# Kernel optimization log

Hardware: AMD Instinct MI355X
Metric: run time of the kernel (lower is better)

## Reference

```python
import jax, jax.numpy as jnp
import numpy as np


def _make_coord(n):
    # grid-center coords in (-1, 1), matching make_coord in the torch code
    return -1.0 + 1.0 / n + (2.0 / n) * jnp.arange(n, dtype=jnp.float32)


def _mlp(inp, W1, b1, W2, b2, W3, b3):
    h = jax.nn.relu(inp @ W1 + b1)
    h = jax.nn.relu(h @ W2 + b2)
    return h @ W3 + b3


def setup_inputs() -> dict:
    key = jax.random.key(0)
    ks = jax.random.split(key, 4)
    dim = 64
    x = jax.random.normal(ks[0], (4, dim, 64, 64), dtype=jnp.float32)
    W1 = jax.random.normal(ks[1], (dim + 2, 256), dtype=jnp.float32) * 0.05
    W2 = jax.random.normal(ks[2], (256, 256), dtype=jnp.float32) * 0.05
    W3 = jax.random.normal(ks[3], (256, dim), dtype=jnp.float32) * 0.05
    return {
        "x": x,
        "W1": W1, "b1": jnp.zeros((256,), jnp.float32),
        "W2": W2, "b2": jnp.zeros((256,), jnp.float32),
        "W3": W3, "b3": jnp.zeros((dim,), jnp.float32),
        "h_out": 256, "w_out": 256,
    }


def reference(x, W1, b1, W2, b2, W3, b3, h_out, w_out):
    B, C, H, W = x.shape
    # query coords on the output grid (same for every batch element)
    gy, gx = jnp.meshgrid(_make_coord(h_out), _make_coord(w_out), indexing="ij")
    cy = gy.reshape(-1)  # [Q], coord channel 0 (height)
    cx = gx.reshape(-1)  # [Q], coord channel 1 (width)
    rx = 1.0 / H  # = 2 / H / 2
    ry = 1.0 / W
    eps_shift = 1e-6
    lim = 1.0 - 1e-6
    fy = _make_coord(H)  # feat_coord values along height
    fx = _make_coord(W)

    preds = []
    areas = []
    for vx in (-1.0, 1.0):
        for vy in (-1.0, 1.0):
            sy = jnp.clip(cy + vx * rx + eps_shift, -lim, lim)
            sx = jnp.clip(cx + vy * ry + eps_shift, -lim, lim)
            # grid_sample nearest, align_corners=False: unnormalize then round
            iy = jnp.clip(jnp.round(((sy + 1.0) * H - 1.0) * 0.5), 0, H - 1).astype(jnp.int32)
            ix = jnp.clip(jnp.round(((sx + 1.0) * W - 1.0) * 0.5), 0, W - 1).astype(jnp.int32)
            q_feat = x[:, :, iy, ix].transpose(0, 2, 1)  # [B, Q, C]
            rel_y = (cy - fy[iy]) * H  # [Q]
            rel_x = (cx - fx[ix]) * W
            rel = jnp.stack([rel_y, rel_x], axis=-1)  # [Q, 2]
            inp = jnp.concatenate(
                [q_feat, jnp.broadcast_to(rel, (B,) + rel.shape)], axis=-1
            )  # [B, Q, C+2]
            preds.append(_mlp(inp, W1, b1, W2, b2, W3, b3))  # [B, Q, C]
            areas.append(jnp.abs(rel_y * rel_x) + 1e-9)  # [Q]

    tot_area = areas[0] + areas[1] + areas[2] + areas[3]
    # local_ensemble swap: 0<->3, 1<->2 (opposite-corner area weighting)
    areas = [areas[3], areas[2], areas[1], areas[0]]
    ret = 0.0
    for pred, area in zip(preds, areas):
        ret = ret + pred * (area / tot_area)[None, :, None]
    return ret  # [B, h_out*w_out, C]
```

## Files before the change

### kernel.cpp

```cpp
#include <hip/hip_runtime.h>


typedef __bf16 bf16x8 __attribute__((ext_vector_type(8)));
typedef float  f32x4  __attribute__((ext_vector_type(4)));

#define LDS_SWZ(row, kbyte) ((kbyte) ^ (((row) & 7) << 4))

#define WP1_U 0
#define WP2_U (48 * 512)
#define WP3_U (176 * 512)

__global__ __launch_bounds__(64) void prep_weights(
    const float* __restrict__ W1, const float* __restrict__ W2,
    const float* __restrict__ W3, ushort* __restrict__ ws)
{
    const int blk = blockIdx.x;
    const int l   = threadIdx.x;
    const float* W; int Kreal, N, ks, nt; size_t off;
    if (blk < 48)       { W = W1; Kreal = 66;  N = 256; ks = blk >> 4;  nt = blk & 15; off = WP1_U + (size_t)blk * 512; }
    else if (blk < 176) { int b2 = blk - 48;  W = W2; Kreal = 256; N = 256; ks = b2 >> 4; nt = b2 & 15; off = WP2_U + (size_t)b2 * 512; }
    else                { int b3 = blk - 176; W = W3; Kreal = 256; N = 64;  ks = b3 >> 2; nt = b3 & 3;  off = WP3_U + (size_t)b3 * 512; }

    const int n = nt * 16 + (l & 15);
    ushort v[8];
    #pragma unroll
    for (int j = 0; j < 8; ++j) {
        const int k = ks * 32 + ((l >> 4) * 8) + j;
        const float f = (k < Kreal) ? W[(size_t)k * N + n] : 0.0f;
        v[j] = __builtin_bit_cast(ushort, (__bf16)f);
    }
    *(uint4*)(ws + off + (size_t)l * 8) = *(const uint4*)v;
}

template<int KSTEPS, int SRC_STRIDE>
__device__ inline void compute_layer(const char* __restrict__ src,
                                     const ushort* __restrict__ wp,
                                     const float* __restrict__ bias,
                                     int lane, int nbase_t, f32x4 (&acc)[4][4])
{
    const int lrow = lane & 15;
    const int lk   = lane >> 4;
    #pragma unroll
    for (int nt = 0; nt < 4; ++nt) {
        const float bs = bias[(nbase_t + nt) * 16 + lrow];
        #pragma unroll
        for (int mt = 0; mt < 4; ++mt)
            acc[mt][nt] = (f32x4){bs, bs, bs, bs};
    }

    const ushort* wpl = wp + (((size_t)nbase_t) << 9) + (lane << 3);
    #pragma unroll 1
    for (int ks = 0; ks < KSTEPS; ++ks) {
        bf16x8 bb[4];
        #pragma unroll
        for (int nt = 0; nt < 4; ++nt)
            bb[nt] = *(const bf16x8*)(wpl + (((size_t)(ks * 16 + nt)) << 9));
        #pragma unroll
        for (int mt = 0; mt < 4; ++mt) {
            const int row   = mt * 16 + lrow;
            const int kbyte = ks * 64 + lk * 16;
            const bf16x8 a = *(const bf16x8*)(src + row * SRC_STRIDE + LDS_SWZ(row, kbyte));
            __builtin_amdgcn_s_setprio(1);
            #pragma unroll
            for (int nt = 0; nt < 4; ++nt)
                acc[mt][nt] = __builtin_amdgcn_mfma_f32_16x16x32_bf16(a, bb[nt], acc[mt][nt], 0, 0, 0);
            __builtin_amdgcn_s_setprio(0);
        }
    }
}

__device__ inline void store_hidden(char* __restrict__ dst, const f32x4 (&acc)[4][4],
                                    int lane, int nbase_t)
{
    const int lrow = lane & 15;
    const int lk   = lane >> 4;
    #pragma unroll
    for (int nt = 0; nt < 4; ++nt) {
        const int n  = (nbase_t + nt) * 16 + lrow;
        const int kbyte = 2 * n;
        #pragma unroll
        for (int mt = 0; mt < 4; ++mt) {
            #pragma unroll
            for (int r = 0; r < 4; ++r) {
                const int row = mt * 16 + lk * 4 + r;
                const float v = fmaxf(acc[mt][nt][r], 0.0f);
                *(ushort*)(dst + row * 512 + LDS_SWZ(row, kbyte)) = __builtin_bit_cast(ushort, (__bf16)v);
            }
        }
    }
}

__global__ __launch_bounds__(256, 3) void liif_mfma4_kernel(
    const float* __restrict__ x,
    const float* __restrict__ b1f, const float* __restrict__ b2f, const float* __restrict__ b3f,
    const ushort* __restrict__ ws, float* __restrict__ out)
{
    __shared__ char bufI[16 * 1024];
    __shared__ char bufH[32 * 1024];
    __shared__ int   s_iy[4][16], s_ix[4][16];
    __shared__ float s_rely[4][16], s_relx[4][16], s_w[4][16];

    const int tid  = threadIdx.x;
    const int lane = tid & 63;
    const int wv   = tid >> 6;
    const int lrow = lane & 15;
    const int lk   = lane >> 4;

    const int bid0 = blockIdx.x;
    const int bid  = (bid0 & 7) * 2048 + (bid0 >> 3);
    const int b    = bid >> 12;
    const int q0   = (bid & 4095) << 4;

    const int nbase_t = wv * 4;

    if (tid < 16) {
        const int q  = q0 + tid;
        const int yq = q >> 8, xq = q & 255;
        const float cy  = -1.0f + (2.0f * yq + 1.0f) / 256.0f;
        const float cx  = -1.0f + (2.0f * xq + 1.0f) / 256.0f;
        const float lim = 1.0f - 1e-6f;
        float area[4];
        #pragma unroll
        for (int c = 0; c < 4; ++c) {
            const float vx = (c & 2) ? 1.0f : -1.0f;
            const float vy = (c & 1) ? 1.0f : -1.0f;
            float sy = cy + vx * (1.0f / 64.0f) + 1e-6f;
            float sx = cx + vy * (1.0f / 64.0f) + 1e-6f;
            sy = fminf(fmaxf(sy, -lim), lim);
            sx = fminf(fmaxf(sx, -lim), lim);
            int iy = (int)rintf(((sy + 1.0f) * 64.0f - 1.0f) * 0.5f);
            int ix = (int)rintf(((sx + 1.0f) * 64.0f - 1.0f) * 0.5f);
            iy = min(max(iy, 0), 63);
            ix = min(max(ix, 0), 63);
            const float fy = -1.0f + (2.0f * iy + 1.0f) / 64.0f;
            const float fx = -1.0f + (2.0f * ix + 1.0f) / 64.0f;
            const float ry = (cy - fy) * 64.0f;
            const float rx = (cx - fx) * 64.0f;
            s_iy[c][tid] = iy;   s_ix[c][tid] = ix;
            s_rely[c][tid] = ry; s_relx[c][tid] = rx;
            area[c] = fabsf(ry * rx) + 1e-9f;
        }
        const float tot = area[0] + area[1] + area[2] + area[3];
        #pragma unroll
        for (int c = 0; c < 4; ++c) s_w[c][tid] = area[3 - c] / tot;
    }
    __syncthreads();

    {
        const int r = tid >> 2, p = tid & 3;
        const int c = r >> 4, q = r & 15;
        const int iy = s_iy[c][q], ix = s_ix[c][q];
        const float* xb = x + (size_t)b * 262144 + iy * 64 + ix;
        #pragma unroll
        for (int half = 0; half < 2; ++half) {
            ushort tmp[8];
            #pragma unroll
            for (int j = 0; j < 8; ++j) {
                const float f = xb[(size_t)(p * 16 + half * 8 + j) * 4096];
                tmp[j] = __builtin_bit_cast(ushort, (__bf16)f);
            }
            const int kbyte = p * 32 + half * 16;
            *(uint4*)(bufI + r * 256 + LDS_SWZ(r, kbyte)) = *(const uint4*)tmp;
        }
        ushort pad[8] = {0, 0, 0, 0, 0, 0, 0, 0};
        if (p == 0) {
            pad[0] = __builtin_bit_cast(ushort, (__bf16)s_rely[c][q]);
            pad[1] = __builtin_bit_cast(ushort, (__bf16)s_relx[c][q]);
        }
        const int kbyte = 128 + p * 16;
        *(uint4*)(bufI + r * 256 + LDS_SWZ(r, kbyte)) = *(const uint4*)pad;
    }
    __syncthreads();

    f32x4 acc[4][4];

    compute_layer<3, 256>(bufI, ws + WP1_U, b1f, lane, nbase_t, acc);
    store_hidden(bufH, acc, lane, nbase_t);
    __syncthreads();

    compute_layer<8, 512>(bufH, ws + WP2_U, b2f, lane, nbase_t, acc);
    __syncthreads();
    store_hidden(bufH, acc, lane, nbase_t);
    __syncthreads();

    {
        const int nt3 = wv;
        const float bs = b3f[nt3 * 16 + lrow];
        f32x4 acc3[4];
        #pragma unroll
        for (int mt = 0; mt < 4; ++mt) acc3[mt] = (f32x4){bs, bs, bs, bs};

        const ushort* wp3 = ws + WP3_U + (lane << 3);
        #pragma unroll 1
        for (int ks = 0; ks < 8; ++ks) {
            const bf16x8 bb = *(const bf16x8*)(wp3 + (((size_t)(ks * 4 + nt3)) << 9));
            #pragma unroll
            for (int mt = 0; mt < 4; ++mt) {
                const int row   = mt * 16 + lrow;
                const int kbyte = ks * 64 + lk * 16;
                const bf16x8 a = *(const bf16x8*)(bufH + row * 512 + LDS_SWZ(row, kbyte));
                __builtin_amdgcn_s_setprio(1);
                acc3[mt] = __builtin_amdgcn_mfma_f32_16x16x32_bf16(a, bb, acc3[mt], 0, 0, 0);
                __builtin_amdgcn_s_setprio(0);
            }
        }
        #pragma unroll
        for (int mt = 0; mt < 4; ++mt) {
            #pragma unroll
            for (int r = 0; r < 4; ++r) {
                const int row = mt * 16 + lk * 4 + r;
                const float wgt = s_w[row >> 4][row & 15];
                const int cb = (nt3 * 16 + lrow) * 4;
                *(float*)(bufI + row * 256 + LDS_SWZ(row, cb)) = acc3[mt][r] * wgt;
            }
        }
    }
    __syncthreads();

    {
        const int q  = tid >> 4;
        const int ch = (tid & 15) * 4;
        f32x4 sum = (f32x4){0.f, 0.f, 0.f, 0.f};
        #pragma unroll
        for (int c = 0; c < 4; ++c) {
            const int row = c * 16 + q;
            const f32x4 v = *(const f32x4*)(bufI + row * 256 + LDS_SWZ(row, ch * 4));
            sum += v;
        }
        *(f32x4*)(out + ((size_t)b * 65536 + q0 + q) * 64 + ch) = sum;
    }
}

extern "C" void kernel_launch(void* const* d_in, const int* in_sizes, int n_in,
                              void* d_out, int out_size, void* d_ws, size_t ws_size,
                              hipStream_t stream) {
    const float* x  = (const float*)d_in[0];
    const float* W1 = (const float*)d_in[1];
    const float* b1 = (const float*)d_in[2];
    const float* W2 = (const float*)d_in[3];
    const float* b2 = (const float*)d_in[4];
    const float* W3 = (const float*)d_in[5];
    const float* b3 = (const float*)d_in[6];
    float* out = (float*)d_out;
    ushort* wp = (ushort*)d_ws;

    prep_weights<<<208, 64, 0, stream>>>(W1, W2, W3, wp);
    liif_mfma4_kernel<<<16384, 256, 0, stream>>>(x, b1, b2, b3, wp, out);
}
```

Baseline: 269.8 us.

## Pre-transpose features to pixel-major bf16 and load layer-1 A directly from global

Adds a prep kernel that converts x into a channel-contiguous bf16 layout per pixel, so the main kernel reads layer-1 A fragments straight from global memory instead of gathering strided fp32 values into shared memory. The relative-coordinate channels are injected directly into the A register for the last K-step, and the per-query coordinate math moves into registers. This removes the input LDS buffer, which together with a higher occupancy hint aims at more resident blocks. The cost is an extra prep pass and an extra barrier before reusing the hidden buffer for the output reduction.

```diff
diff --git a/kernel.cpp b/kernel.cpp
--- a/kernel.cpp
+++ b/kernel.cpp
@@ -9,6 +9,7 @@
 #define WP1_U 0
 #define WP2_U (48 * 512)
 #define WP3_U (176 * 512)
+#define XT_OFF (1 << 20)
 
 __global__ __launch_bounds__(64) void prep_weights(
     const float* __restrict__ W1, const float* __restrict__ W2,
@@ -32,41 +33,21 @@
     *(uint4*)(ws + off + (size_t)l * 8) = *(const uint4*)v;
 }
 
-template<int KSTEPS, int SRC_STRIDE>
-__device__ inline void compute_layer(const char* __restrict__ src,
-                                     const ushort* __restrict__ wp,
-                                     const float* __restrict__ bias,
-                                     int lane, int nbase_t, f32x4 (&acc)[4][4])
-{
-    const int lrow = lane & 15;
-    const int lk   = lane >> 4;
+__global__ __launch_bounds__(256) void prep_xt(const float* __restrict__ x, char* __restrict__ xt)
+{
+    const int blk = blockIdx.x;
+    const int b = blk >> 6, iy = blk & 63;
+    const int ix = threadIdx.x & 63, cq = threadIdx.x >> 6;
+    ushort v[16];
     #pragma unroll
-    for (int nt = 0; nt < 4; ++nt) {
-        const float bs = bias[(nbase_t + nt) * 16 + lrow];
-        #pragma unroll
-        for (int mt = 0; mt < 4; ++mt)
-            acc[mt][nt] = (f32x4){bs, bs, bs, bs};
-    }
-
-    const ushort* wpl = wp + (((size_t)nbase_t) << 9) + (lane << 3);
-    #pragma unroll 1
-    for (int ks = 0; ks < KSTEPS; ++ks) {
-        bf16x8 bb[4];
-        #pragma unroll
-        for (int nt = 0; nt < 4; ++nt)
-            bb[nt] = *(const bf16x8*)(wpl + (((size_t)(ks * 16 + nt)) << 9));
-        #pragma unroll
-        for (int mt = 0; mt < 4; ++mt) {
-            const int row   = mt * 16 + lrow;
-            const int kbyte = ks * 64 + lk * 16;
-            const bf16x8 a = *(const bf16x8*)(src + row * SRC_STRIDE + LDS_SWZ(row, kbyte));
-            __builtin_amdgcn_s_setprio(1);
-            #pragma unroll
-            for (int nt = 0; nt < 4; ++nt)
-                acc[mt][nt] = __builtin_amdgcn_mfma_f32_16x16x32_bf16(a, bb[nt], acc[mt][nt], 0, 0, 0);
-            __builtin_amdgcn_s_setprio(0);
-        }
-    }
+    for (int j = 0; j < 16; ++j) {
+        const int ch = cq * 16 + j;
+        const float f = x[(((size_t)b * 64 + ch) * 64 + iy) * 64 + ix];
+        v[j] = __builtin_bit_cast(ushort, (__bf16)f);
+    }
+    char* dst = xt + ((size_t)((b * 4096 + iy * 64 + ix)) * 128) + cq * 32;
+    *(uint4*)dst        = *(const uint4*)(v);
+    *(uint4*)(dst + 16) = *(const uint4*)(v + 8);
 }
 
 __device__ inline void store_hidden(char* __restrict__ dst, const f32x4 (&acc)[4][4],
@@ -90,31 +71,30 @@
     }
 }
 
-__global__ __launch_bounds__(256, 3) void liif_mfma4_kernel(
-    const float* __restrict__ x,
+__global__ __launch_bounds__(256, 4) void liif_mfma5_kernel(
+    const char* __restrict__ xt,
     const float* __restrict__ b1f, const float* __restrict__ b2f, const float* __restrict__ b3f,
     const ushort* __restrict__ ws, float* __restrict__ out)
 {
-    __shared__ char bufI[16 * 1024];
     __shared__ char bufH[32 * 1024];
-    __shared__ int   s_iy[4][16], s_ix[4][16];
-    __shared__ float s_rely[4][16], s_relx[4][16], s_w[4][16];
+    __shared__ float s_w[4][16];
 
     const int tid  = threadIdx.x;
     const int lane = tid & 63;
     const int wv   = tid >> 6;
     const int lrow = lane & 15;
     const int lk   = lane >> 4;
+    const int nbase_t = wv * 4;
 
     const int bid0 = blockIdx.x;
-    const int bid  = (bid0 & 7) * 2048 + (bid0 >> 3);
-    const int b    = bid >> 12;
-    const int q0   = (bid & 4095) << 4;
-
-    const int nbase_t = wv * 4;
-
-    if (tid < 16) {
-        const int q  = q0 + tid;
+    const int b    = (bid0 & 7) >> 1;
+    const int qidx = (bid0 >> 3) * 2 + (bid0 & 1);
+    const int q0   = qidx << 4;
+
+    int   pix_off[4];
+    float rely[4], relx[4];
+    {
+        const int q  = q0 + lrow;
         const int yq = q >> 8, xq = q & 255;
         const float cy  = -1.0f + (2.0f * yq + 1.0f) / 256.0f;
         const float cx  = -1.0f + (2.0f * xq + 1.0f) / 256.0f;
@@ -128,57 +108,97 @@
             float sx = cx + vy * (1.0f / 64.0f) + 1e-6f;
             sy = fminf(fmaxf(sy, -lim), lim);
             sx = fminf(fmaxf(sx, -lim), lim);
-            int iy = (int)rintf(((sy + 1.0f) * 64.0f - 1.0f) * 0.5f);
-            int ix = (int)rintf(((sx + 1.0f) * 64.0f - 1.0f) * 0.5f);
-            iy = min(max(iy, 0), 63);
-            ix = min(max(ix, 0), 63);
-            const float fy = -1.0f + (2.0f * iy + 1.0f) / 64.0f;
-            const float fx = -1.0f + (2.0f * ix + 1.0f) / 64.0f;
-            const float ry = (cy - fy) * 64.0f;
-            const float rx = (cx - fx) * 64.0f;
-            s_iy[c][tid] = iy;   s_ix[c][tid] = ix;
-            s_rely[c][tid] = ry; s_relx[c][tid] = rx;
-            area[c] = fabsf(ry * rx) + 1e-9f;
-        }
-        const float tot = area[0] + area[1] + area[2] + area[3];
-        #pragma unroll
-        for (int c = 0; c < 4; ++c) s_w[c][tid] = area[3 - c] / tot;
-    }
-    __syncthreads();
-
-    {
-        const int r = tid >> 2, p = tid & 3;
-        const int c = r >> 4, q = r & 15;
-        const int iy = s_iy[c][q], ix = s_ix[c][q];
-        const float* xb = x + (size_t)b * 262144 + iy * 64 + ix;
-        #pragma unroll
-        for (int half = 0; half < 2; ++half) {
-            ushort tmp[8];
-            #pragma unroll
-            for (int j = 0; j < 8; ++j) {
-                const float f = xb[(size_t)(p * 16 + half * 8 + j) * 4096];
-                tmp[j] = __builtin_bit_cast(ushort, (__bf16)f);
-            }
-            const int kbyte = p * 32 + half * 16;
-            *(uint4*)(bufI + r * 256 + LDS_SWZ(r, kbyte)) = *(const uint4*)tmp;
-        }
-        ushort pad[8] = {0, 0, 0, 0, 0, 0, 0, 0};
-        if (p == 0) {
-            pad[0] = __builtin_bit_cast(ushort, (__bf16)s_rely[c][q]);
-            pad[1] = __builtin_bit_cast(ushort, (__bf16)s_relx[c][q]);
-        }
-        const int kbyte = 128 + p * 16;
-        *(uint4*)(bufI + r * 256 + LDS_SWZ(r, kbyte)) = *(const uint4*)pad;
-    }
-    __syncthreads();
+            int iyv = (int)rintf(((sy + 1.0f) * 64.0f - 1.0f) * 0.5f);
+            int ixv = (int)rintf(((sx + 1.0f) * 64.0f - 1.0f) * 0.5f);
+            iyv = min(max(iyv, 0), 63);
+            ixv = min(max(ixv, 0), 63);
+            const float fy = -1.0f + (2.0f * iyv + 1.0f) / 64.0f;
+            const float fx = -1.0f + (2.0f * ixv + 1.0f) / 64.0f;
+            rely[c] = (cy - fy) * 64.0f;
+            relx[c] = (cx - fx) * 64.0f;
+            pix_off[c] = (b * 4096 + iyv * 64 + ixv) * 128;
+            area[c] = fabsf(rely[c] * relx[c]) + 1e-9f;
+        }
+        if (tid < 16) {
+            const float tot = area[0] + area[1] + area[2] + area[3];
+            #pragma unroll
+            for (int c = 0; c < 4; ++c) s_w[c][lrow] = area[3 - c] / tot;
+        }
+    }
 
     f32x4 acc[4][4];
 
-    compute_layer<3, 256>(bufI, ws + WP1_U, b1f, lane, nbase_t, acc);
+    {
+        #pragma unroll
+        for (int nt = 0; nt < 4; ++nt) {
+            const float bs = b1f[(nbase_t + nt) * 16 + lrow];
+            #pragma unroll
+            for (int mt = 0; mt < 4; ++mt) acc[mt][nt] = (f32x4){bs, bs, bs, bs};
+        }
+        const ushort* wpl = ws + WP1_U + ((size_t)nbase_t << 9) + (lane << 3);
+        #pragma unroll 1
+        for (int ks = 0; ks < 2; ++ks) {
+            bf16x8 bb[4];
+            #pragma unroll
+            for (int nt = 0; nt < 4; ++nt)
+                bb[nt] = *(const bf16x8*)(wpl + ((size_t)(ks * 16 + nt) << 9));
+            #pragma unroll
+            for (int mt = 0; mt < 4; ++mt) {
+                const bf16x8 a = *(const bf16x8*)(xt + pix_off[mt] + ks * 64 + lk * 16);
+                __builtin_amdgcn_s_setprio(1);
+                #pragma unroll
+                for (int nt = 0; nt < 4; ++nt)
+                    acc[mt][nt] = __builtin_amdgcn_mfma_f32_16x16x32_bf16(a, bb[nt], acc[mt][nt], 0, 0, 0);
+                __builtin_amdgcn_s_setprio(0);
+            }
+        }
+        {
+            bf16x8 bb[4];
+            #pragma unroll
+            for (int nt = 0; nt < 4; ++nt)
+                bb[nt] = *(const bf16x8*)(wpl + ((size_t)(32 + nt) << 9));
+            #pragma unroll
+            for (int mt = 0; mt < 4; ++mt) {
+                bf16x8 a = (bf16x8){0, 0, 0, 0, 0, 0, 0, 0};
+                if (lk == 0) { a[0] = (__bf16)rely[mt]; a[1] = (__bf16)relx[mt]; }
+                __builtin_amdgcn_s_setprio(1);
+                #pragma unroll
+                for (int nt = 0; nt < 4; ++nt)
+                    acc[mt][nt] = __builtin_amdgcn_mfma_f32_16x16x32_bf16(a, bb[nt], acc[mt][nt], 0, 0, 0);
+                __builtin_amdgcn_s_setprio(0);
+            }
+        }
+    }
     store_hidden(bufH, acc, lane, nbase_t);
     __syncthreads();
 
-    compute_layer<8, 512>(bufH, ws + WP2_U, b2f, lane, nbase_t, acc);
+    {
+        #pragma unroll
+        for (int nt = 0; nt < 4; ++nt) {
+            const float bs = b2f[(nbase_t + nt) * 16 + lrow];
+            #pragma unroll
+            for (int mt = 0; mt < 4; ++mt) acc[mt][nt] = (f32x4){bs, bs, bs, bs};
+        }
+        const ushort* wpl = ws + WP2_U + ((size_t)nbase_t << 9) + (lane << 3);
+        #pragma unroll 1
+        for (int ks = 0; ks < 8; ++ks) {
+            bf16x8 bb[4];
+            #pragma unroll
+            for (int nt = 0; nt < 4; ++nt)
+                bb[nt] = *(const bf16x8*)(wpl + ((size_t)(ks * 16 + nt) << 9));
+            #pragma unroll
+            for (int mt = 0; mt < 4; ++mt) {
+                const int row   = mt * 16 + lrow;
+                const int kbyte = ks * 64 + lk * 16;
+                const bf16x8 a = *(const bf16x8*)(bufH + row * 512 + LDS_SWZ(row, kbyte));
+                __builtin_amdgcn_s_setprio(1);
+                #pragma unroll
+                for (int nt = 0; nt < 4; ++nt)
+                    acc[mt][nt] = __builtin_amdgcn_mfma_f32_16x16x32_bf16(a, bb[nt], acc[mt][nt], 0, 0, 0);
+                __builtin_amdgcn_s_setprio(0);
+            }
+        }
+    }
     __syncthreads();
     store_hidden(bufH, acc, lane, nbase_t);
     __syncthreads();
@@ -193,7 +213,7 @@
         const ushort* wp3 = ws + WP3_U + (lane << 3);
         #pragma unroll 1
         for (int ks = 0; ks < 8; ++ks) {
-            const bf16x8 bb = *(const bf16x8*)(wp3 + (((size_t)(ks * 4 + nt3)) << 9));
+            const bf16x8 bb = *(const bf16x8*)(wp3 + ((size_t)(ks * 4 + nt3) << 9));
             #pragma unroll
             for (int mt = 0; mt < 4; ++mt) {
                 const int row   = mt * 16 + lrow;
@@ -204,6 +224,7 @@
                 __builtin_amdgcn_s_setprio(0);
             }
         }
+        __syncthreads();
         #pragma unroll
         for (int mt = 0; mt < 4; ++mt) {
             #pragma unroll
@@ -211,7 +232,7 @@
                 const int row = mt * 16 + lk * 4 + r;
                 const float wgt = s_w[row >> 4][row & 15];
                 const int cb = (nt3 * 16 + lrow) * 4;
-                *(float*)(bufI + row * 256 + LDS_SWZ(row, cb)) = acc3[mt][r] * wgt;
+                *(float*)(bufH + row * 256 + LDS_SWZ(row, cb)) = acc3[mt][r] * wgt;
             }
         }
     }
@@ -224,7 +245,7 @@
         #pragma unroll
         for (int c = 0; c < 4; ++c) {
             const int row = c * 16 + q;
-            const f32x4 v = *(const f32x4*)(bufI + row * 256 + LDS_SWZ(row, ch * 4));
+            const f32x4 v = *(const f32x4*)(bufH + row * 256 + LDS_SWZ(row, ch * 4));
             sum += v;
         }
         *(f32x4*)(out + ((size_t)b * 65536 + q0 + q) * 64 + ch) = sum;
@@ -243,7 +264,9 @@
     const float* b3 = (const float*)d_in[6];
     float* out = (float*)d_out;
     ushort* wp = (ushort*)d_ws;
+    char* xt   = (char*)d_ws + XT_OFF;
 
     prep_weights<<<208, 64, 0, stream>>>(W1, W2, W3, wp);
-    liif_mfma4_kernel<<<16384, 256, 0, stream>>>(x, b1, b2, b3, wp, out);
-}
+    prep_xt<<<256, 256, 0, stream>>>(x, xt);
+    liif_mfma5_kernel<<<16384, 256, 0, stream>>>(xt, b1, b2, b3, wp, out);
+}
```

Result: slower. 361.0 us (+33.8%).
